# Kernel optimization log

Hardware: AMD Instinct MI355X
Metric: run time of the kernel (lower is better)

## Reference

```python
import jax, jax.numpy as jnp
import numpy as np


def setup_inputs() -> dict:
    key = jax.random.key(0)
    B, C, H, W = 16, 128, 64, 64
    k = 3
    x = jax.random.normal(key, (B, C, H, W), dtype=jnp.float32)
    # Fixed identity 'im2col' kernel: eye(k*k) -> (k*k, 1, k, k), non-trainable buffer.
    weights = jnp.eye(k * k, dtype=jnp.float32).reshape(k * k, 1, k, k)
    return {"x": x, "weights": weights}


def reference(x, weights):
    B, C, H, W = x.shape
    k = weights.shape[-1]  # kernel_size
    pad = k // 2
    # Treat every (b, c) plane as an independent single-channel image.
    xr = x.reshape(B * C, 1, H, W)
    # Eye-weighted conv == unfold: each of the k*k output channels is a shifted copy.
    y = jax.lax.conv_general_dilated(
        xr, weights,
        window_strides=(1, 1),
        padding=((pad, pad), (pad, pad)),
        dimension_numbers=("NCHW", "OIHW", "NCHW"),
    )  # (B*C, k*k, H, W)
    return y.reshape(B, C * k * k, H * W)
```

## Files before the change

### kernel.cpp

```cpp
#include <hip/hip_runtime.h>


#define HW_BITS 12
#define W_BITS  6
#define PLANE_W 64
#define PLANE_H 64

typedef float f32x4 __attribute__((ext_vector_type(4)));

__global__ __launch_bounds__(256) void unfold_kernel(
    const float* __restrict__ x, float* __restrict__ y, int total4) {
    int i = blockIdx.x * blockDim.x + threadIdx.x;
    if (i >= total4) return;

    int p     = i << 2;
    int pix   = p & ((1 << HW_BITS) - 1);
    int plane = p >> HW_BITS;
    int h = pix >> W_BITS;
    int w = pix & (PLANE_W - 1);

    int t  = plane % 9;
    int bc = plane / 9;
    int dh = t / 3 - 1;
    int dw = t % 3 - 1;

    int row = h + dh;
    f32x4 v = (f32x4)(0.f, 0.f, 0.f, 0.f);
    if (row >= 0 && row < PLANE_H) {
        const float* src = x + ((size_t)bc << HW_BITS) + ((size_t)row << W_BITS);
        int c0 = w + dw;
        v.x = (c0 >= 0)              ? src[c0]     : 0.f;
        v.y =                          src[c0 + 1];
        v.z =                          src[c0 + 2];
        v.w = (c0 + 3 < PLANE_W)     ? src[c0 + 3] : 0.f;
    }
    __builtin_nontemporal_store(v, ((f32x4*)y) + i);
}

extern "C" void kernel_launch(void* const* d_in, const int* in_sizes, int n_in,
                              void* d_out, int out_size, void* d_ws, size_t ws_size,
                              hipStream_t stream) {
    const float* x = (const float*)d_in[0];
    float* y = (float*)d_out;

    int total4 = out_size >> 2;
    int block = 256;
    int grid = (total4 + block - 1) / block;
    unfold_kernel<<<grid, block, 0, stream>>>(x, y, total4);
}
```

Baseline: 350.8 us.

## Stage each plane in padded LDS tile and emit nine shifted copies

Each block now loads one full 64x64 plane into a zero-padded shared-memory tile with coalesced vector loads. It then writes all nine shifted output channels from LDS, replacing per-output global gathers and branchy boundary checks. This removes redundant global reads and index math, at the cost of LDS zero-fill, barriers and scalar LDS reads. The nontemporal store hint is dropped.

```diff
diff --git a/kernel.cpp b/kernel.cpp
--- a/kernel.cpp
+++ b/kernel.cpp
@@ -1,40 +1,49 @@
 #include <hip/hip_runtime.h>
 
 
-#define HW_BITS 12
-#define W_BITS  6
-#define PLANE_W 64
-#define PLANE_H 64
+#define LDS_STRIDE 67
+#define LDS_ELEMS (66 * LDS_STRIDE)
 
 typedef float f32x4 __attribute__((ext_vector_type(4)));
 
 __global__ __launch_bounds__(256) void unfold_kernel(
-    const float* __restrict__ x, float* __restrict__ y, int total4) {
-    int i = blockIdx.x * blockDim.x + threadIdx.x;
-    if (i >= total4) return;
+    const float* __restrict__ x, float* __restrict__ y) {
+    __shared__ float lds[LDS_ELEMS];
+    const int j  = threadIdx.x;
+    const int bc = blockIdx.x;
 
-    int p     = i << 2;
-    int pix   = p & ((1 << HW_BITS) - 1);
-    int plane = p >> HW_BITS;
-    int h = pix >> W_BITS;
-    int w = pix & (PLANE_W - 1);
+    for (int s = j; s < LDS_ELEMS; s += 256) lds[s] = 0.f;
+    __syncthreads();
 
-    int t  = plane % 9;
-    int bc = plane / 9;
-    int dh = t / 3 - 1;
-    int dw = t % 3 - 1;
+    const f32x4* plane = (const f32x4*)(x + ((size_t)bc << 12));
+    #pragma unroll
+    for (int q = 0; q < 4; ++q) {
+        int f = q * 256 + j;
+        f32x4 v = plane[f];
+        int h = f >> 4;
+        int w = (f & 15) << 2;
+        float* dst = &lds[(h + 1) * LDS_STRIDE + (w + 1)];
+        dst[0] = v.x; dst[1] = v.y; dst[2] = v.z; dst[3] = v.w;
+    }
+    __syncthreads();
 
-    int row = h + dh;
-    f32x4 v = (f32x4)(0.f, 0.f, 0.f, 0.f);
-    if (row >= 0 && row < PLANE_H) {
-        const float* src = x + ((size_t)bc << HW_BITS) + ((size_t)row << W_BITS);
-        int c0 = w + dw;
-        v.x = (c0 >= 0)              ? src[c0]     : 0.f;
-        v.y =                          src[c0 + 1];
-        v.z =                          src[c0 + 2];
-        v.w = (c0 + 3 < PLANE_W)     ? src[c0 + 3] : 0.f;
+    float* ybase = y + ((size_t)bc * 9 << 12);
+    #pragma unroll
+    for (int t = 0; t < 9; ++t) {
+        const int dh = t / 3 - 1;
+        const int dw = t % 3 - 1;
+        f32x4* yt = (f32x4*)(ybase + ((size_t)t << 12));
+        #pragma unroll
+        for (int q = 0; q < 4; ++q) {
+            int f = q * 256 + j;
+            int h = f >> 4;
+            int w = (f & 15) << 2;
+            const float* s = &lds[(h + 1 + dh) * LDS_STRIDE + (w + 1 + dw)];
+            f32x4 v;
+            v.x = s[0]; v.y = s[1]; v.z = s[2]; v.w = s[3];
+            yt[f] = v;
+        }
     }
-    __builtin_nontemporal_store(v, ((f32x4*)y) + i);
 }
 
 extern "C" void kernel_launch(void* const* d_in, const int* in_sizes, int n_in,
@@ -43,8 +52,5 @@
     const float* x = (const float*)d_in[0];
     float* y = (float*)d_out;
 
-    int total4 = out_size >> 2;
-    int block = 256;
-    int grid = (total4 + block - 1) / block;
-    unfold_kernel<<<grid, block, 0, stream>>>(x, y, total4);
+    unfold_kernel<<<2048, 256, 0, stream>>>(x, y);
 }
```

Measured after the change: 326.8 us. 6.8% less time.
